# Performance work log

Measured on AMD Instinct MI355X. Metric: run time of the kernel, lower is better.

Reference implementation:

```python
import jax, jax.numpy as jnp
import numpy as np

H = 128           # hidden_dim
N = 20000         # num_nucleotides
APN = 22          # atoms per nucleotide
A = N * APN       # total atoms
PHYS = 10         # INVARIANT_PHYSICS_DIM


def setup_inputs() -> dict:
    key = jax.random.key(0)
    ks = jax.random.split(key, 12)
    w = lambda k, shape: jax.random.normal(k, shape, dtype=jnp.float32) * 0.05
    return {
        "physics_x": jax.random.normal(ks[0], (A, PHYS), dtype=jnp.float32),
        "learnable_emb": jax.random.normal(ks[1], (A, H), dtype=jnp.float32),
        "atom_to_nuc": (jnp.arange(A) // APN).astype(jnp.int32),  # sorted, every segment non-empty
        "sugar_x": jax.random.normal(ks[2], (N, 8), dtype=jnp.float32),
        "phos_x": jax.random.normal(ks[3], (N, 8), dtype=jnp.float32),
        "num_nucleotides": N,
        # parameters (stored [in, out]; same math as torch Linear)
        "sugar_W": w(ks[4], (8, H)), "sugar_b": jnp.zeros((H,), jnp.float32),
        "phos_W": w(ks[5], (8, H)), "phos_b": jnp.zeros((H,), jnp.float32),
        "attn_W1": w(ks[6], (PHYS + H, H)), "attn_b1": jnp.zeros((H,), jnp.float32),
        "attn_W2": w(ks[7], (H, 1)), "attn_b2": jnp.zeros((1,), jnp.float32),
        "comb_W": w(ks[8], (3 * H, H)), "comb_b": jnp.zeros((H,), jnp.float32),
        "ln_g": jnp.ones((H,), jnp.float32), "ln_b": jnp.zeros((H,), jnp.float32),
        "rot_W1": w(ks[9], (H, H)), "rot_b1": jnp.zeros((H,), jnp.float32),
        "rot_W2": jnp.zeros((H, 4), jnp.float32), "rot_b2": jnp.array([1.0, 0.0, 0.0, 0.0], jnp.float32),
        "tr_W1": w(ks[10], (H, H)), "tr_b1": jnp.zeros((H,), jnp.float32),
        "tr_W2": jnp.zeros((H, 3), jnp.float32), "tr_b2": jnp.zeros((3,), jnp.float32),
    }


def reference(physics_x, learnable_emb, atom_to_nuc, sugar_x, phos_x, num_nucleotides,
              sugar_W, sugar_b, phos_W, phos_b, attn_W1, attn_b1, attn_W2, attn_b2,
              comb_W, comb_b, ln_g, ln_b, rot_W1, rot_b1, rot_W2, rot_b2,
              tr_W1, tr_b1, tr_W2, tr_b2):
    h_sugar = sugar_x @ sugar_W + sugar_b            # [N, H]
    h_phos = phos_x @ phos_W + phos_b                # [N, H]

    full = jnp.concatenate([physics_x, learnable_emb], axis=-1)  # [A, PHYS+H]
    s = (jnp.tanh(full @ attn_W1 + attn_b1) @ attn_W2 + attn_b2)[:, 0]  # [A] attention logits

    # segment softmax over atoms of each nucleotide (replaces the per-nuc Python loop)
    m = jax.ops.segment_max(s, atom_to_nuc, num_segments=num_nucleotides, indices_are_sorted=True)
    e = jnp.exp(s - m[atom_to_nuc])
    den = jax.ops.segment_sum(e, atom_to_nuc, num_segments=num_nucleotides, indices_are_sorted=True)
    w = e / den[atom_to_nuc]                          # [A]
    pooled = jax.ops.segment_sum(w[:, None] * learnable_emb, atom_to_nuc,
                                 num_segments=num_nucleotides, indices_are_sorted=True)  # [N, H]

    z = jnp.concatenate([pooled, h_sugar, h_phos], axis=-1) @ comb_W + comb_b  # [N, H]
    mu = z.mean(axis=-1, keepdims=True)
    var = z.var(axis=-1, keepdims=True)
    zn = (z - mu) / jnp.sqrt(var + 1e-5) * ln_g + ln_b
    nuc_emb = zn * jax.nn.sigmoid(zn)                 # SiLU

    q = jax.nn.silu(nuc_emb @ rot_W1 + rot_b1) @ rot_W2 + rot_b2  # [N, 4]
    quaternions = q / jnp.maximum(jnp.linalg.norm(q, axis=-1, keepdims=True), 1e-12)
    translations = jax.nn.silu(nuc_emb @ tr_W1 + tr_b1) @ tr_W2 + tr_b2  # [N, 3]
    return (quaternions, translations, nuc_emb)
```

## Files before the change

### kernel.cpp

```cpp
#include <hip/hip_runtime.h>

typedef unsigned short u16;
typedef unsigned int   u32;
typedef short bf16x8 __attribute__((ext_vector_type(8)));
typedef float f32x4 __attribute__((ext_vector_type(4)));

#define APN   22
#define NBK   8
#define AB    176
#define EMBS  136

__device__ __forceinline__ float bflo(u32 u){ return __uint_as_float(u << 16); }
__device__ __forceinline__ float bfhi(u32 u){ return __uint_as_float(u & 0xffff0000u); }
__device__ __forceinline__ u16 f2bf(float f){
  u32 u = __float_as_uint(f);
  u32 r = u + 0x7fffu + ((u >> 16) & 1u);
  return (u16)(r >> 16);
}
__device__ __forceinline__ u32 pack2(float a, float b){
  return (u32)f2bf(a) | ((u32)f2bf(b) << 16);
}
__device__ __forceinline__ float wave_sum(float v){
  #pragma unroll
  for (int off = 32; off; off >>= 1) v += __shfl_xor(v, off, 64);
  return v;
}
__device__ __forceinline__ float fast_tanh(float x){
  float t = __expf(-2.f * x);
  return 2.f * __builtin_amdgcn_rcpf(1.f + t) - 1.f;
}
__device__ __forceinline__ float silu_f(float x){
  return x * __builtin_amdgcn_rcpf(1.f + __expf(-x));
}

__global__ void k_prep_w1(const float* __restrict__ W1, u32* __restrict__ bfrag32)
{
  const int b = blockIdx.x;
  const int ks = b >> 3, t = b & 7;
  const int e0 = threadIdx.x * 2;
  const int lane = e0 >> 3, j = e0 & 7;
  const int n = t * 16 + (lane & 15);
  float v[2];
  #pragma unroll
  for (int i = 0; i < 2; ++i) {
    int kp = ks * 32 + ((lane >> 4) * 8) + j + i;
    float val = 0.f;
    if (kp < 128)       val = W1[(size_t)(10 + kp) * 128 + n];
    else if (kp < 138)  val = W1[(size_t)(kp - 128) * 128 + n];
    v[i] = val;
  }
  bfrag32[((size_t)(b * 64 + lane)) * 4 + (j >> 1)] = pack2(v[0], v[1]);
}

__global__ void k_prep_frag3(const float* __restrict__ combW, const float* __restrict__ rotW1,
                             const float* __restrict__ trW1,
                             u32* __restrict__ combF, u32* __restrict__ rotF, u32* __restrict__ trF)
{
  const int b = blockIdx.x;
  const float* W; u32* outp; int rel;
  if (b < 96)       { W = combW; outp = combF; rel = b; }
  else if (b < 128) { W = rotW1; outp = rotF;  rel = b - 96; }
  else              { W = trW1;  outp = trF;   rel = b - 128; }
  const int ks = rel >> 3, t = rel & 7;
  const int e0 = threadIdx.x * 2;
  const int lane = e0 >> 3, j = e0 & 7;
  const int n = t * 16 + (lane & 15);
  const int k = ks * 32 + ((lane >> 4) * 8) + j;
  outp[((size_t)(rel * 64 + lane)) * 4 + (j >> 1)] =
      pack2(W[(size_t)k * 128 + n], W[(size_t)(k + 1) * 128 + n]);
}

__global__ __launch_bounds__(256, 3) void k_fused(
    const float* __restrict__ phys, const float* __restrict__ emb,
    const float* __restrict__ b1, const float* __restrict__ W2,
    const uint4* __restrict__ bfragG,
    float* __restrict__ pooled, int A, int N)
{
  __shared__ u16 embt[AB][EMBS];
  __shared__ float s_part[4][AB];
  __shared__ float w_lds[AB];

  const int tid  = threadIdx.x;
  const int lane = tid & 63;
  const int wv   = tid >> 6;
  const int a0   = blockIdx.x * AB;
  const int q = lane >> 4, nn = lane & 15;

  bf16x8 bb[5][2];
  #pragma unroll
  for (int ks = 0; ks < 5; ++ks)
    #pragma unroll
    for (int u = 0; u < 2; ++u)
      bb[ks][u] = ((const bf16x8*)bfragG)[(ks * 8 + wv * 2 + u) * 64 + lane];

  float b1v[2], w2v[2];
  #pragma unroll
  for (int u = 0; u < 2; ++u) {
    int j = (wv * 2 + u) * 16 + nn;
    b1v[u] = b1[j]; w2v[u] = W2[j];
  }

  #pragma unroll
  for (int it = 0; it < (AB * 16) / 256; ++it) {
    int c = it * 256 + tid;
    int row = c >> 4, seg = c & 15;
    int ga = a0 + row;
    float4 v0 = make_float4(0.f, 0.f, 0.f, 0.f), v1 = v0;
    if (ga < A) {
      const float4* src = (const float4*)&emb[(size_t)ga * 128 + seg * 8];
      v0 = src[0]; v1 = src[1];
    }
    *(uint4*)&embt[row][seg * 8] =
        make_uint4(pack2(v0.x, v0.y), pack2(v0.z, v0.w),
                   pack2(v1.x, v1.y), pack2(v1.z, v1.w));
  }
  __syncthreads();

  #pragma unroll 2
  for (int tile = 0; tile < 11; ++tile) {
    const int m  = tile * 16 + nn;
    const int ga = a0 + m;
    union { u32 u[4]; bf16x8 v; } apu;
    #pragma unroll
    for (int i = 0; i < 4; ++i) {
      int c = q * 8 + i * 2;
      float2 pv = make_float2(0.f, 0.f);
      if (ga < A && c < 10) pv = *(const float2*)&phys[(size_t)ga * 10 + c];
      apu.u[i] = pack2(pv.x, pv.y);
    }
    f32x4 acc0 = (f32x4){0.f, 0.f, 0.f, 0.f};
    f32x4 acc1 = (f32x4){0.f, 0.f, 0.f, 0.f};
    #pragma unroll
    for (int ks = 0; ks < 4; ++ks) {
      bf16x8 af = *(const bf16x8*)&embt[m][ks * 32 + q * 8];
      acc0 = __builtin_amdgcn_mfma_f32_16x16x32_bf16(af, bb[ks][0], acc0, 0, 0, 0);
      acc1 = __builtin_amdgcn_mfma_f32_16x16x32_bf16(af, bb[ks][1], acc1, 0, 0, 0);
    }
    acc0 = __builtin_amdgcn_mfma_f32_16x16x32_bf16(apu.v, bb[4][0], acc0, 0, 0, 0);
    acc1 = __builtin_amdgcn_mfma_f32_16x16x32_bf16(apu.v, bb[4][1], acc1, 0, 0, 0);

    #pragma unroll
    for (int r = 0; r < 4; ++r) {
      float a = fast_tanh(acc0[r] + b1v[0]) * w2v[0]
              + fast_tanh(acc1[r] + b1v[1]) * w2v[1];
      #pragma unroll
      for (int off = 1; off < 16; off <<= 1) a += __shfl_xor(a, off, 64);
      if (nn == 0) s_part[wv][tile * 16 + q * 4 + r] = a;
    }
  }
  __syncthreads();

  {
    int seg = lane >> 5, id = lane & 31;
    int nl = wv * 2 + seg;
    int nuc = blockIdx.x * NBK + nl;
    bool act = (id < APN) && (nuc < N);
    int idx = nl * APN + id;
    float sv = act ? (s_part[0][idx] + s_part[1][idx] + s_part[2][idx] + s_part[3][idx])
                   : -3.0e38f;
    float mx = sv;
    #pragma unroll
    for (int off = 16; off; off >>= 1) mx = fmaxf(mx, __shfl_xor(mx, off, 32));
    float e = act ? __expf(sv - mx) : 0.f;
    float den = e;
    #pragma unroll
    for (int off = 16; off; off >>= 1) den += __shfl_xor(den, off, 32);
    if (id < APN) w_lds[idx] = e / den;
  }
  __syncthreads();

  {
    int nl = tid >> 5, t32 = tid & 31;
    int nuc = blockIdx.x * NBK + nl;
    if (nuc < N) {
      float o0 = 0.f, o1 = 0.f, o2 = 0.f, o3 = 0.f;
      int base = nl * APN;
      #pragma unroll 2
      for (int a = 0; a < APN; ++a) {
        float wa = w_lds[base + a];
        uint2 u = *(const uint2*)&embt[base + a][t32 * 4];
        o0 += wa * bflo(u.x); o1 += wa * bfhi(u.x);
        o2 += wa * bflo(u.y); o3 += wa * bfhi(u.y);
      }
      *(float4*)&pooled[(size_t)nuc * 128 + t32 * 4] = make_float4(o0, o1, o2, o3);
    }
  }
}

__global__ __launch_bounds__(256, 2) void k_combine(
    const float* __restrict__ pooled,
    const float* __restrict__ sugar_x, const float* __restrict__ phos_x,
    const float* __restrict__ sugarW, const float* __restrict__ sugarB,
    const float* __restrict__ phosW, const float* __restrict__ phosB,
    const uint4* __restrict__ combF, const float* __restrict__ combB,
    const float* __restrict__ lng, const float* __restrict__ lnb,
    const uint4* __restrict__ rotF, const float* __restrict__ rotB1,
    const float* __restrict__ rotW2, const float* __restrict__ rotB2,
    const uint4* __restrict__ trF, const float* __restrict__ trB1,
    const float* __restrict__ trW2, const float* __restrict__ trB2,
    float* __restrict__ out, int N)
{
  __shared__ u16 xbuf[64 * 392];
  __shared__ u16 bsl[2][8][64][8];

  const int tid  = threadIdx.x;
  const int lane = tid & 63;
  const int wv   = tid >> 6;
  const int nn   = lane & 15, q = lane >> 4;
  const int nb   = blockIdx.x * 64;
  const size_t t_off  = (size_t)N * 4;
  const size_t ne_off = (size_t)N * 7;

  {
    const int j0 = lane * 2;
    float2 sBv = *(const float2*)&sugarB[j0];
    float2 pBv = *(const float2*)&phosB[j0];
    float2 swv[8], pwv[8];
    #pragma unroll
    for (int k = 0; k < 8; ++k) {
      swv[k] = *(const float2*)&sugarW[(size_t)k * 128 + j0];
      pwv[k] = *(const float2*)&phosW[(size_t)k * 128 + j0];
    }
    #pragma unroll 1
    for (int n = 0; n < 16; ++n) {
      int row = wv * 16 + n, nuc = nb + row;
      u32 up = 0, us = 0, uq = 0;
      if (nuc < N) {
        float2 pl  = ((const float2*)pooled)[(size_t)nuc * 64 + lane];
        float4 sa  = *(const float4*)&sugar_x[(size_t)nuc * 8];
        float4 sb4 = *(const float4*)&sugar_x[(size_t)nuc * 8 + 4];
        float4 pa  = *(const float4*)&phos_x[(size_t)nuc * 8];
        float4 pb4 = *(const float4*)&phos_x[(size_t)nuc * 8 + 4];
        float hs0 = sBv.x + sa.x*swv[0].x + sa.y*swv[1].x + sa.z*swv[2].x + sa.w*swv[3].x
                          + sb4.x*swv[4].x + sb4.y*swv[5].x + sb4.z*swv[6].x + sb4.w*swv[7].x;
        float hs1 = sBv.y + sa.x*swv[0].y + sa.y*swv[1].y + sa.z*swv[2].y + sa.w*swv[3].y
                          + sb4.x*swv[4].y + sb4.y*swv[5].y + sb4.z*swv[6].y + sb4.w*swv[7].y;
        float hp0 = pBv.x + pa.x*pwv[0].x + pa.y*pwv[1].x + pa.z*pwv[2].x + pa.w*pwv[3].x
                          + pb4.x*pwv[4].x + pb4.y*pwv[5].x + pb4.z*pwv[6].x + pb4.w*pwv[7].x;
        float hp1 = pBv.y + pa.x*pwv[0].y + pa.y*pwv[1].y + pa.z*pwv[2].y + pa.w*pwv[3].y
                          + pb4.x*pwv[4].y + pb4.y*pwv[5].y + pb4.z*pwv[6].y + pb4.w*pwv[7].y;
        up = pack2(pl.x, pl.y); us = pack2(hs0, hs1); uq = pack2(hp0, hp1);
      }
      *(u32*)&xbuf[row * 392 +       j0] = up;
      *(u32*)&xbuf[row * 392 + 128 + j0] = us;
      *(u32*)&xbuf[row * 392 + 256 + j0] = uq;
    }
  }
  {
    uint4 p0 = combF[tid * 2], p1 = combF[tid * 2 + 1];
    ((uint4*)&bsl[0][0][0][0])[tid * 2]     = p0;
    ((uint4*)&bsl[0][0][0][0])[tid * 2 + 1] = p1;
  }
  __syncthreads();

  f32x4 acc[8];
  #pragma unroll
  for (int t = 0; t < 8; ++t) acc[t] = (f32x4){0.f, 0.f, 0.f, 0.f};

  const int arow = wv * 16 + nn;
  for (int ks = 0; ks < 12; ++ks) {
    const int buf = ks & 1;
    uint4 n0, n1;
    if (ks < 11) {
      n0 = combF[(ks + 1) * 512 + tid * 2];
      n1 = combF[(ks + 1) * 512 + tid * 2 + 1];
    }
    bf16x8 af = *(const bf16x8*)&xbuf[arow * 392 + ks * 32 + q * 8];
    #pragma unroll
    for (int t = 0; t < 8; ++t) {
      bf16x8 bb = *(const bf16x8*)&bsl[buf][t][lane][0];
      acc[t] = __builtin_amdgcn_mfma_f32_16x16x32_bf16(af, bb, acc[t], 0, 0, 0);
    }
    if (ks < 11) {
      ((uint4*)&bsl[buf ^ 1][0][0][0])[tid * 2]     = n0;
      ((uint4*)&bsl[buf ^ 1][0][0][0])[tid * 2 + 1] = n1;
    }
    __syncthreads();
  }

  {
    float gt[8], bt[8], cbv[8];
    #pragma unroll
    for (int t = 0; t < 8; ++t) {
      gt[t] = lng[t * 16 + nn]; bt[t] = lnb[t * 16 + nn]; cbv[t] = combB[t * 16 + nn];
    }
    #pragma unroll
    for (int r = 0; r < 4; ++r) {
      float z[8]; float s1 = 0.f, s2 = 0.f;
      #pragma unroll
      for (int t = 0; t < 8; ++t) {
        z[t] = acc[t][r] + cbv[t];
        s1 += z[t]; s2 += z[t] * z[t];
      }
      #pragma unroll
      for (int off = 1; off < 16; off <<= 1) {
        s1 += __shfl_xor(s1, off, 64);
        s2 += __shfl_xor(s2, off, 64);
      }
      float mu   = s1 * 0.0078125f;
      float var  = s2 * 0.0078125f - mu * mu;
      float rstd = rsqrtf(var + 1e-5f);
      int row = q * 4 + r, nuc = nb + wv * 16 + row;
      #pragma unroll
      for (int t = 0; t < 8; ++t) {
        float zn = (z[t] - mu) * rstd * gt[t] + bt[t];
        float ne = silu_f(zn);
        if (nuc < N) out[ne_off + (size_t)nuc * 128 + t * 16 + nn] = ne;
        xbuf[(wv * 16 + row) * 136 + t * 16 + nn] = f2bf(ne);
      }
    }
  }
  __syncthreads();

  f32x4 racc[8], tacc[8];
  #pragma unroll
  for (int t = 0; t < 8; ++t) { racc[t] = (f32x4){0.f,0.f,0.f,0.f}; tacc[t] = (f32x4){0.f,0.f,0.f,0.f}; }
  #pragma unroll
  for (int ks = 0; ks < 4; ++ks) {
    bf16x8 af = *(const bf16x8*)&xbuf[arow * 136 + ks * 32 + q * 8];
    #pragma unroll
    for (int t = 0; t < 8; ++t) {
      bf16x8 rb = ((const bf16x8*)rotF)[(ks * 8 + t) * 64 + lane];
      bf16x8 tb = ((const bf16x8*)trF)[(ks * 8 + t) * 64 + lane];
      racc[t] = __builtin_amdgcn_mfma_f32_16x16x32_bf16(af, rb, racc[t], 0, 0, 0);
      tacc[t] = __builtin_amdgcn_mfma_f32_16x16x32_bf16(af, tb, tacc[t], 0, 0, 0);
    }
  }

  {
    float rb1[8], tb1[8], twx[8], twy[8], twz[8]; float4 rw2[8];
    #pragma unroll
    for (int t = 0; t < 8; ++t) {
      int j = t * 16 + nn;
      rb1[t] = rotB1[j]; tb1[t] = trB1[j];
      rw2[t] = *(const float4*)&rotW2[(size_t)j * 4];
      twx[t] = trW2[(size_t)j * 3]; twy[t] = trW2[(size_t)j * 3 + 1]; twz[t] = trW2[(size_t)j * 3 + 2];
    }
    float qb0 = rotB2[0], qb1 = rotB2[1], qb2 = rotB2[2], qb3 = rotB2[3];
    float pb0 = trB2[0], pb1 = trB2[1], pb2 = trB2[2];
    #pragma unroll
    for (int r = 0; r < 4; ++r) {
      float q0=0.f,q1=0.f,q2=0.f,q3=0.f,p0=0.f,p1=0.f,p2=0.f;
      #pragma unroll
      for (int t = 0; t < 8; ++t) {
        float u = silu_f(racc[t][r] + rb1[t]);
        float v = silu_f(tacc[t][r] + tb1[t]);
        q0 += u * rw2[t].x; q1 += u * rw2[t].y; q2 += u * rw2[t].z; q3 += u * rw2[t].w;
        p0 += v * twx[t];   p1 += v * twy[t];   p2 += v * twz[t];
      }
      #pragma unroll
      for (int off = 1; off < 16; off <<= 1) {
        q0 += __shfl_xor(q0, off, 64); q1 += __shfl_xor(q1, off, 64);
        q2 += __shfl_xor(q2, off, 64); q3 += __shfl_xor(q3, off, 64);
        p0 += __shfl_xor(p0, off, 64); p1 += __shfl_xor(p1, off, 64);
        p2 += __shfl_xor(p2, off, 64);
      }
      int nuc = nb + wv * 16 + q * 4 + r;
      if (nn == 0 && nuc < N) {
        q0 += qb0; q1 += qb1; q2 += qb2; q3 += qb3;
        float nrm = fmaxf(sqrtf(q0*q0 + q1*q1 + q2*q2 + q3*q3), 1e-12f);
        float inv = 1.f / nrm;
        out[(size_t)nuc * 4 + 0] = q0 * inv;
        out[(size_t)nuc * 4 + 1] = q1 * inv;
        out[(size_t)nuc * 4 + 2] = q2 * inv;
        out[(size_t)nuc * 4 + 3] = q3 * inv;
        out[t_off + (size_t)nuc * 3 + 0] = p0 + pb0;
        out[t_off + (size_t)nuc * 3 + 1] = p1 + pb1;
        out[t_off + (size_t)nuc * 3 + 2] = p2 + pb2;
      }
    }
  }
}

extern "C" void kernel_launch(void* const* d_in, const int* in_sizes, int n_in,
                              void* d_out, int out_size, void* d_ws, size_t ws_size,
                              hipStream_t stream) {
  const float* phys    = (const float*)d_in[0];
  const float* emb     = (const float*)d_in[1];
  const float* sugar_x = (const float*)d_in[3];
  const float* phos_x  = (const float*)d_in[4];
  const float* sugarW  = (const float*)d_in[6];
  const float* sugarB  = (const float*)d_in[7];
  const float* phosW   = (const float*)d_in[8];
  const float* phosB   = (const float*)d_in[9];
  const float* attnW1  = (const float*)d_in[10];
  const float* attnB1  = (const float*)d_in[11];
  const float* attnW2  = (const float*)d_in[12];
  const float* combW   = (const float*)d_in[14];
  const float* combB   = (const float*)d_in[15];
  const float* lng     = (const float*)d_in[16];
  const float* lnb     = (const float*)d_in[17];
  const float* rotW1   = (const float*)d_in[18];
  const float* rotB1   = (const float*)d_in[19];
  const float* rotW2   = (const float*)d_in[20];
  const float* rotB2   = (const float*)d_in[21];
  const float* trW1    = (const float*)d_in[22];
  const float* trB1    = (const float*)d_in[23];
  const float* trW2    = (const float*)d_in[24];
  const float* trB2    = (const float*)d_in[25];

  const int A = in_sizes[2];
  const int N = in_sizes[3] / 8;

  char* ws = (char*)d_ws;
  u32*   bfragW1 = (u32*)ws;
  u32*   combF   = (u32*)(ws + 40960);
  u32*   rotF    = (u32*)(ws + 139264);
  u32*   trF     = (u32*)(ws + 172032);
  float* pooled  = (float*)(ws + 204800);

  k_prep_w1<<<40, 256, 0, stream>>>(attnW1, bfragW1);
  k_prep_frag3<<<160, 256, 0, stream>>>(combW, rotW1, trW1, combF, rotF, trF);
  k_fused<<<(N + NBK - 1) / NBK, 256, 0, stream>>>(
      phys, emb, attnB1, attnW2, (const uint4*)bfragW1, pooled, A, N);
  k_combine<<<(N + 63) / 64, 256, 0, stream>>>(
      pooled, sugar_x, phos_x, sugarW, sugarB, phosW, phosB,
      (const uint4*)combF, combB, lng, lnb,
      (const uint4*)rotF, rotB1, rotW2, rotB2,
      (const uint4*)trF, trB1, trW2, trB2,
      (float*)d_out, N);
}
```

Measured before the change: 456.5 us.

## Stream fp32 embedding K-slices via direct global-to-LDS loads with double buffering

Replaces the up-front fp32-to-bf16 conversion of the whole embedding tile into padded LDS with four 32-column fp32 K-slices. Each slice is loaded with global_load_lds into an XOR-swizzled double buffer, so the next slice's load overlaps MFMAs on the current one. Operands are converted with v_cvt_pk_bf16_f32, and 22 accumulators are held in registers across all K steps. The pooling stage now re-reads the fp32 embeddings from global memory (likely cache-resident) instead of LDS. This raises register pressure and adds one barrier per K step.

Result: slower. 481.0 us (+5.4%).

```diff
diff --git a/kernel.cpp b/kernel.cpp
--- a/kernel.cpp
+++ b/kernel.cpp
@@ -8,7 +8,6 @@
 #define APN   22
 #define NBK   8
 #define AB    176
-#define EMBS  136
 
 __device__ __forceinline__ float bflo(u32 u){ return __uint_as_float(u << 16); }
 __device__ __forceinline__ float bfhi(u32 u){ return __uint_as_float(u & 0xffff0000u); }
@@ -20,6 +19,11 @@
 __device__ __forceinline__ u32 pack2(float a, float b){
   return (u32)f2bf(a) | ((u32)f2bf(b) << 16);
 }
+__device__ __forceinline__ u32 cvtpk(float lo, float hi){
+  u32 d;
+  asm volatile("v_cvt_pk_bf16_f32 %0, %1, %2" : "=v"(d) : "v"(lo), "v"(hi));
+  return d;
+}
 __device__ __forceinline__ float wave_sum(float v){
   #pragma unroll
   for (int off = 32; off; off >>= 1) v += __shfl_xor(v, off, 64);
@@ -31,6 +35,11 @@
 }
 __device__ __forceinline__ float silu_f(float x){
   return x * __builtin_amdgcn_rcpf(1.f + __expf(-x));
+}
+__device__ __forceinline__ void gl_lds16(const float* g, const void* l){
+  __builtin_amdgcn_global_load_lds(
+      (const __attribute__((address_space(1))) void*)g,
+      (__attribute__((address_space(3))) void*)l, 16, 0, 0);
 }
 
 __global__ void k_prep_w1(const float* __restrict__ W1, u32* __restrict__ bfrag32)
@@ -76,7 +85,7 @@
     const uint4* __restrict__ bfragG,
     float* __restrict__ pooled, int A, int N)
 {
-  __shared__ u16 embt[AB][EMBS];
+  __shared__ float4 eslice[2][1408];
   __shared__ float s_part[4][AB];
   __shared__ float w_lds[AB];
 
@@ -85,67 +94,93 @@
   const int wv   = tid >> 6;
   const int a0   = blockIdx.x * AB;
   const int q = lane >> 4, nn = lane & 15;
-
-  bf16x8 bb[5][2];
-  #pragma unroll
-  for (int ks = 0; ks < 5; ++ks)
-    #pragma unroll
-    for (int u = 0; u < 2; ++u)
-      bb[ks][u] = ((const bf16x8*)bfragG)[(ks * 8 + wv * 2 + u) * 64 + lane];
-
-  float b1v[2], w2v[2];
-  #pragma unroll
-  for (int u = 0; u < 2; ++u) {
-    int j = (wv * 2 + u) * 16 + nn;
-    b1v[u] = b1[j]; w2v[u] = W2[j];
-  }
-
-  #pragma unroll
-  for (int it = 0; it < (AB * 16) / 256; ++it) {
-    int c = it * 256 + tid;
-    int row = c >> 4, seg = c & 15;
-    int ga = a0 + row;
-    float4 v0 = make_float4(0.f, 0.f, 0.f, 0.f), v1 = v0;
-    if (ga < A) {
-      const float4* src = (const float4*)&emb[(size_t)ga * 128 + seg * 8];
-      v0 = src[0]; v1 = src[1];
-    }
-    *(uint4*)&embt[row][seg * 8] =
-        make_uint4(pack2(v0.x, v0.y), pack2(v0.z, v0.w),
-                   pack2(v1.x, v1.y), pack2(v1.z, v1.w));
-  }
+  const bf16x8* bfbf = (const bf16x8*)bfragG;
+
+  #pragma unroll
+  for (int k = 0; k < 6; ++k) {
+    int c = k * 256 + tid;
+    if (c < 1408) {
+      int r = c >> 3, g = c & 7;
+      int row = a0 + r; if (row >= A) row = A - 1;
+      const float* gp = emb + (size_t)row * 128 + (g ^ (r & 7)) * 4;
+      gl_lds16(gp, (const void*)&eslice[0][c]);
+    }
+  }
+
+  bf16x8 bbc0 = bfbf[(0 * 8 + wv * 2 + 0) * 64 + lane];
+  bf16x8 bbc1 = bfbf[(0 * 8 + wv * 2 + 1) * 64 + lane];
+  float b1v0, b1v1, w2v0, w2v1;
+  {
+    int j0 = (wv * 2) * 16 + nn, j1 = (wv * 2 + 1) * 16 + nn;
+    b1v0 = b1[j0]; b1v1 = b1[j1]; w2v0 = W2[j0]; w2v1 = W2[j1];
+  }
+
+  f32x4 accA[11], accB[11];
+  #pragma unroll
+  for (int t = 0; t < 11; ++t) {
+    accA[t] = (f32x4){0.f, 0.f, 0.f, 0.f};
+    accB[t] = (f32x4){0.f, 0.f, 0.f, 0.f};
+  }
+
   __syncthreads();
 
+  for (int ks = 0; ks < 4; ++ks) {
+    const int buf = ks & 1;
+    if (ks < 3) {
+      #pragma unroll
+      for (int k = 0; k < 6; ++k) {
+        int c = k * 256 + tid;
+        if (c < 1408) {
+          int r = c >> 3, g = c & 7;
+          int row = a0 + r; if (row >= A) row = A - 1;
+          const float* gp = emb + (size_t)row * 128 + (ks + 1) * 32 + (g ^ (r & 7)) * 4;
+          gl_lds16(gp, (const void*)&eslice[buf ^ 1][c]);
+        }
+      }
+    }
+    bf16x8 nb0 = bfbf[((ks + 1) * 8 + wv * 2 + 0) * 64 + lane];
+    bf16x8 nb1 = bfbf[((ks + 1) * 8 + wv * 2 + 1) * 64 + lane];
+
+    #pragma unroll
+    for (int t = 0; t < 11; ++t) {
+      const int m = t * 16 + nn;
+      const float4* rowp = &eslice[buf][m * 8];
+      float4 A0 = rowp[(2 * q)     ^ (m & 7)];
+      float4 A1 = rowp[(2 * q + 1) ^ (m & 7)];
+      union { u32 u[4]; bf16x8 v; } af;
+      af.u[0] = cvtpk(A0.x, A0.y); af.u[1] = cvtpk(A0.z, A0.w);
+      af.u[2] = cvtpk(A1.x, A1.y); af.u[3] = cvtpk(A1.z, A1.w);
+      accA[t] = __builtin_amdgcn_mfma_f32_16x16x32_bf16(af.v, bbc0, accA[t], 0, 0, 0);
+      accB[t] = __builtin_amdgcn_mfma_f32_16x16x32_bf16(af.v, bbc1, accB[t], 0, 0, 0);
+    }
+    bbc0 = nb0; bbc1 = nb1;
+    __syncthreads();
+  }
+
   #pragma unroll 2
-  for (int tile = 0; tile < 11; ++tile) {
-    const int m  = tile * 16 + nn;
-    const int ga = a0 + m;
-    union { u32 u[4]; bf16x8 v; } apu;
+  for (int t = 0; t < 11; ++t) {
+    const int m = t * 16 + nn, ga = a0 + m;
+    union { u32 u[4]; bf16x8 v; } ap;
     #pragma unroll
     for (int i = 0; i < 4; ++i) {
       int c = q * 8 + i * 2;
       float2 pv = make_float2(0.f, 0.f);
       if (ga < A && c < 10) pv = *(const float2*)&phys[(size_t)ga * 10 + c];
-      apu.u[i] = pack2(pv.x, pv.y);
-    }
-    f32x4 acc0 = (f32x4){0.f, 0.f, 0.f, 0.f};
-    f32x4 acc1 = (f32x4){0.f, 0.f, 0.f, 0.f};
-    #pragma unroll
-    for (int ks = 0; ks < 4; ++ks) {
-      bf16x8 af = *(const bf16x8*)&embt[m][ks * 32 + q * 8];
-      acc0 = __builtin_amdgcn_mfma_f32_16x16x32_bf16(af, bb[ks][0], acc0, 0, 0, 0);
-      acc1 = __builtin_amdgcn_mfma_f32_16x16x32_bf16(af, bb[ks][1], acc1, 0, 0, 0);
-    }
-    acc0 = __builtin_amdgcn_mfma_f32_16x16x32_bf16(apu.v, bb[4][0], acc0, 0, 0, 0);
-    acc1 = __builtin_amdgcn_mfma_f32_16x16x32_bf16(apu.v, bb[4][1], acc1, 0, 0, 0);
-
+      ap.u[i] = cvtpk(pv.x, pv.y);
+    }
+    accA[t] = __builtin_amdgcn_mfma_f32_16x16x32_bf16(ap.v, bbc0, accA[t], 0, 0, 0);
+    accB[t] = __builtin_amdgcn_mfma_f32_16x16x32_bf16(ap.v, bbc1, accB[t], 0, 0, 0);
+  }
+
+  #pragma unroll
+  for (int t = 0; t < 11; ++t) {
     #pragma unroll
     for (int r = 0; r < 4; ++r) {
-      float a = fast_tanh(acc0[r] + b1v[0]) * w2v[0]
-              + fast_tanh(acc1[r] + b1v[1]) * w2v[1];
+      float a = fast_tanh(accA[t][r] + b1v0) * w2v0
+              + fast_tanh(accB[t][r] + b1v1) * w2v1;
       #pragma unroll
       for (int off = 1; off < 16; off <<= 1) a += __shfl_xor(a, off, 64);
-      if (nn == 0) s_part[wv][tile * 16 + q * 4 + r] = a;
+      if (nn == 0) s_part[wv][t * 16 + q * 4 + r] = a;
     }
   }
   __syncthreads();
@@ -178,9 +213,8 @@
       #pragma unroll 2
       for (int a = 0; a < APN; ++a) {
         float wa = w_lds[base + a];
-        uint2 u = *(const uint2*)&embt[base + a][t32 * 4];
-        o0 += wa * bflo(u.x); o1 += wa * bfhi(u.x);
-        o2 += wa * bflo(u.y); o3 += wa * bfhi(u.y);
+        float4 e = *(const float4*)&emb[(size_t)(a0 + base + a) * 128 + t32 * 4];
+        o0 += wa * e.x; o1 += wa * e.y; o2 += wa * e.z; o3 += wa * e.w;
       }
       *(float4*)&pooled[(size_t)nuc * 128 + t32 * 4] = make_float4(o0, o1, o2, o3);
     }
```

## Load MFMA A-fragments directly from global with double-buffered tile prefetch

Applied to the files above, without the earlier changes.

Instead of staging the whole embedding block into LDS and then reading the A fragments back, each wave now loads its own fp32 rows straight from global memory into registers. It double-buffers the next tile's loads behind the current tile's MFMA and tanh work, converts with the hardware v_cvt_pk_bf16_f32 instruction, and writes only one quarter of the bf16 tile to LDS per wave for later pooling. This removes the upfront load-then-sync barrier and the LDS round trip, so memory latency can overlap compute. The cost is more registers, with launch bounds lowered from 3 to 2 blocks per CU. Each embedding row is also redundantly loaded by all four waves, relying on cache hits.

Measured after the change: 434.2 us. -4.9%, faster.

```diff
diff --git a/kernel.cpp b/kernel.cpp
--- a/kernel.cpp
+++ b/kernel.cpp
@@ -19,6 +19,11 @@
 }
 __device__ __forceinline__ u32 pack2(float a, float b){
   return (u32)f2bf(a) | ((u32)f2bf(b) << 16);
+}
+__device__ __forceinline__ u32 cvtpk(float lo, float hi){
+  u32 d;
+  asm volatile("v_cvt_pk_bf16_f32 %0, %1, %2" : "=v"(d) : "v"(lo), "v"(hi));
+  return d;
 }
 __device__ __forceinline__ float wave_sum(float v){
   #pragma unroll
@@ -70,7 +75,47 @@
       pack2(W[(size_t)k * 128 + n], W[(size_t)(k + 1) * 128 + n]);
 }
 
-__global__ __launch_bounds__(256, 3) void k_fused(
+struct EBuf { float4 e[8]; float2 p[4]; };
+
+__device__ __forceinline__ void load_tile(EBuf& b, const float* __restrict__ emb,
+                                          const float* __restrict__ phys,
+                                          int a0, int t, int nn, int q, int A)
+{
+  int ga = a0 + t * 16 + nn;
+  int row = (ga < A) ? ga : (A - 1);
+  const float* rp = emb + (size_t)row * 128 + q * 8;
+  #pragma unroll
+  for (int ks = 0; ks < 4; ++ks) {
+    b.e[ks * 2]     = *(const float4*)(rp + ks * 32);
+    b.e[ks * 2 + 1] = *(const float4*)(rp + ks * 32 + 4);
+  }
+  const float* pp = phys + (size_t)row * 10 + q * 8;
+  #pragma unroll
+  for (int i = 0; i < 4; ++i) {
+    int c = q * 8 + 2 * i;
+    b.p[i] = (c < 10) ? *(const float2*)(pp + 2 * i) : make_float2(0.f, 0.f);
+  }
+}
+
+__device__ __forceinline__ void conv_tile(const EBuf& b, bf16x8 af[5])
+{
+  union { u32 u[4]; bf16x8 v; } w;
+  #pragma unroll
+  for (int ks = 0; ks < 4; ++ks) {
+    w.u[0] = cvtpk(b.e[ks*2].x,   b.e[ks*2].y);
+    w.u[1] = cvtpk(b.e[ks*2].z,   b.e[ks*2].w);
+    w.u[2] = cvtpk(b.e[ks*2+1].x, b.e[ks*2+1].y);
+    w.u[3] = cvtpk(b.e[ks*2+1].z, b.e[ks*2+1].w);
+    af[ks] = w.v;
+  }
+  w.u[0] = cvtpk(b.p[0].x, b.p[0].y);
+  w.u[1] = cvtpk(b.p[1].x, b.p[1].y);
+  w.u[2] = cvtpk(b.p[2].x, b.p[2].y);
+  w.u[3] = cvtpk(b.p[3].x, b.p[3].y);
+  af[4] = w.v;
+}
+
+__global__ __launch_bounds__(256, 2) void k_fused(
     const float* __restrict__ phys, const float* __restrict__ emb,
     const float* __restrict__ b1, const float* __restrict__ W2,
     const uint4* __restrict__ bfragG,
@@ -85,67 +130,53 @@
   const int wv   = tid >> 6;
   const int a0   = blockIdx.x * AB;
   const int q = lane >> 4, nn = lane & 15;
-
-  bf16x8 bb[5][2];
-  #pragma unroll
-  for (int ks = 0; ks < 5; ++ks)
-    #pragma unroll
-    for (int u = 0; u < 2; ++u)
-      bb[ks][u] = ((const bf16x8*)bfragG)[(ks * 8 + wv * 2 + u) * 64 + lane];
-
-  float b1v[2], w2v[2];
-  #pragma unroll
-  for (int u = 0; u < 2; ++u) {
-    int j = (wv * 2 + u) * 16 + nn;
-    b1v[u] = b1[j]; w2v[u] = W2[j];
-  }
-
-  #pragma unroll
-  for (int it = 0; it < (AB * 16) / 256; ++it) {
-    int c = it * 256 + tid;
-    int row = c >> 4, seg = c & 15;
-    int ga = a0 + row;
-    float4 v0 = make_float4(0.f, 0.f, 0.f, 0.f), v1 = v0;
-    if (ga < A) {
-      const float4* src = (const float4*)&emb[(size_t)ga * 128 + seg * 8];
-      v0 = src[0]; v1 = src[1];
-    }
-    *(uint4*)&embt[row][seg * 8] =
-        make_uint4(pack2(v0.x, v0.y), pack2(v0.z, v0.w),
-                   pack2(v1.x, v1.y), pack2(v1.z, v1.w));
-  }
-  __syncthreads();
-
-  #pragma unroll 2
-  for (int tile = 0; tile < 11; ++tile) {
-    const int m  = tile * 16 + nn;
-    const int ga = a0 + m;
-    union { u32 u[4]; bf16x8 v; } apu;
-    #pragma unroll
-    for (int i = 0; i < 4; ++i) {
-      int c = q * 8 + i * 2;
-      float2 pv = make_float2(0.f, 0.f);
-      if (ga < A && c < 10) pv = *(const float2*)&phys[(size_t)ga * 10 + c];
-      apu.u[i] = pack2(pv.x, pv.y);
-    }
-    f32x4 acc0 = (f32x4){0.f, 0.f, 0.f, 0.f};
-    f32x4 acc1 = (f32x4){0.f, 0.f, 0.f, 0.f};
-    #pragma unroll
-    for (int ks = 0; ks < 4; ++ks) {
-      bf16x8 af = *(const bf16x8*)&embt[m][ks * 32 + q * 8];
-      acc0 = __builtin_amdgcn_mfma_f32_16x16x32_bf16(af, bb[ks][0], acc0, 0, 0, 0);
-      acc1 = __builtin_amdgcn_mfma_f32_16x16x32_bf16(af, bb[ks][1], acc1, 0, 0, 0);
-    }
-    acc0 = __builtin_amdgcn_mfma_f32_16x16x32_bf16(apu.v, bb[4][0], acc0, 0, 0, 0);
-    acc1 = __builtin_amdgcn_mfma_f32_16x16x32_bf16(apu.v, bb[4][1], acc1, 0, 0, 0);
+  const bf16x8* bfbf = (const bf16x8*)bfragG;
+
+  bf16x8 bbA[5], bbB[5];
+  #pragma unroll
+  for (int ks = 0; ks < 5; ++ks) {
+    bbA[ks] = bfbf[(ks * 8 + wv * 2 + 0) * 64 + lane];
+    bbB[ks] = bfbf[(ks * 8 + wv * 2 + 1) * 64 + lane];
+  }
+  float b1v0, b1v1, w2v0, w2v1;
+  {
+    int j0 = (wv * 2) * 16 + nn, j1 = (wv * 2 + 1) * 16 + nn;
+    b1v0 = b1[j0]; b1v1 = b1[j1]; w2v0 = W2[j0]; w2v1 = W2[j1];
+  }
+
+  EBuf eb[2];
+  load_tile(eb[0], emb, phys, a0, 0, nn, q, A);
+
+  #pragma unroll
+  for (int t = 0; t < 11; ++t) {
+    if (t < 10) load_tile(eb[(t + 1) & 1], emb, phys, a0, t + 1, nn, q, A);
+
+    bf16x8 af[5];
+    conv_tile(eb[t & 1], af);
+
+    {
+      u16* dst = &embt[t * 16 + nn][q * 8];
+      if      (wv == 0) *(bf16x8*)(dst +  0) = af[0];
+      else if (wv == 1) *(bf16x8*)(dst + 32) = af[1];
+      else if (wv == 2) *(bf16x8*)(dst + 64) = af[2];
+      else              *(bf16x8*)(dst + 96) = af[3];
+    }
+
+    f32x4 accA = (f32x4){0.f, 0.f, 0.f, 0.f};
+    f32x4 accB = (f32x4){0.f, 0.f, 0.f, 0.f};
+    #pragma unroll
+    for (int ks = 0; ks < 5; ++ks) {
+      accA = __builtin_amdgcn_mfma_f32_16x16x32_bf16(af[ks], bbA[ks], accA, 0, 0, 0);
+      accB = __builtin_amdgcn_mfma_f32_16x16x32_bf16(af[ks], bbB[ks], accB, 0, 0, 0);
+    }
 
     #pragma unroll
     for (int r = 0; r < 4; ++r) {
-      float a = fast_tanh(acc0[r] + b1v[0]) * w2v[0]
-              + fast_tanh(acc1[r] + b1v[1]) * w2v[1];
+      float a = fast_tanh(accA[r] + b1v0) * w2v0
+              + fast_tanh(accB[r] + b1v1) * w2v1;
       #pragma unroll
       for (int off = 1; off < 16; off <<= 1) a += __shfl_xor(a, off, 64);
-      if (nn == 0) s_part[wv][tile * 16 + q * 4 + r] = a;
+      if (nn == 0) s_part[wv][t * 16 + q * 4 + r] = a;
     }
   }
   __syncthreads();
```
